# Kernel optimization log

Measured on AMD Instinct MI355X. Metric: run time of the kernel, lower is better.

Reference implementation:

```python
import jax, jax.numpy as jnp
import numpy as np

DT = 0.01        # base_dt from __init__
DT_SCALE = 1.0   # forward default


def setup_inputs() -> dict:
    key = jax.random.key(0)
    k1, k2, k3, k4, k5 = jax.random.split(key, 5)
    B, D, R = 4096, 512, 128
    x = jax.random.normal(k1, (B, D), dtype=jnp.float32)
    v = jax.random.normal(k2, (B, D), dtype=jnp.float32)
    force = jax.random.normal(k3, (B, D), dtype=jnp.float32)
    U = jax.random.normal(k4, (D, R), dtype=jnp.float32) * (1.0 / np.sqrt(D))
    W = jax.random.normal(k5, (R, D), dtype=jnp.float32) * (1.0 / np.sqrt(R))
    return {"x": x, "v": v, "force": force, "U": U, "W": W, "steps": 8}


def reference(x, v, force, U, W, steps):
    dt = DT * DT_SCALE
    # Dormand-Prince (DP5) tableau
    a21 = 1/5
    a31, a32 = 3/40, 9/40
    a41, a42, a43 = 44/45, -56/15, 32/9
    a51, a52, a53, a54 = 19372/6561, -25360/2187, 64448/6561, -212/729
    a61, a62, a63, a64, a65 = 9017/3168, -355/33, 46732/5247, 49/176, -5103/18656
    b1, b3, b4, b5, b6 = 35/384, 500/1113, 125/192, -2187/6784, 11/84

    def dynamics(tx, tv):
        # low-rank Christoffel: gamma(v, x) = ((v @ U) * (x @ U)) @ W
        acc = -jnp.einsum('br,rd->bd', (tv @ U) * (tx @ U), W)
        return acc + force

    def step(carry, _):
        cx, cv = carry
        k1x = cv
        k1v = dynamics(cx, cv)
        x2 = cx + dt * (a21 * k1x); v2 = cv + dt * (a21 * k1v)
        k2x = v2; k2v = dynamics(x2, v2)
        x3 = cx + dt * (a31 * k1x + a32 * k2x)
        v3 = cv + dt * (a31 * k1v + a32 * k2v)
        k3x = v3; k3v = dynamics(x3, v3)
        x4 = cx + dt * (a41 * k1x + a42 * k2x + a43 * k3x)
        v4 = cv + dt * (a41 * k1v + a42 * k2v + a43 * k3v)
        k4x = v4; k4v = dynamics(x4, v4)
        x5 = cx + dt * (a51 * k1x + a52 * k2x + a53 * k3x + a54 * k4x)
        v5 = cv + dt * (a51 * k1v + a52 * k2v + a53 * k3v + a54 * k4v)
        k5x = v5; k5v = dynamics(x5, v5)
        x6 = cx + dt * (a61 * k1x + a62 * k2x + a63 * k3x + a64 * k4x + a65 * k5x)
        v6 = cv + dt * (a61 * k1v + a62 * k2v + a63 * k3v + a64 * k4v + a65 * k5v)
        k6x = v6; k6v = dynamics(x6, v6)
        nx = cx + dt * (b1 * k1x + b3 * k3x + b4 * k4x + b5 * k5x + b6 * k6x)
        nv = cv + dt * (b1 * k1v + b3 * k3v + b4 * k4v + b5 * k5v + b6 * k6v)
        return (nx, nv), None

    (fx, fv), _ = jax.lax.scan(step, (x, v), None, length=steps)
    return fx, fv
```

## Files before the change

kernel.cpp:

```cpp
#include <hip/hip_runtime.h>


typedef _Float16 v8h __attribute__((ext_vector_type(8)));
typedef float v4f __attribute__((ext_vector_type(4)));
typedef unsigned short u16;
typedef unsigned int u32;

#define MFMAH __builtin_amdgcn_mfma_f32_16x16x32_f16
#define INV2048 4.8828125e-4f
#define INV256  0.00390625f
#define SSTR 144

__device__ __forceinline__ float swap8(float x){
  return __int_as_float(
    __builtin_amdgcn_mov_dpp(__float_as_int(x), 0x128, 0xf, 0xf, true));
}

struct Tab {
  double a[7][7]; double b[7]; double A[7]; double XC[7][7]; double XF[7]; double cxc[7];
};
static constexpr Tab make_tab() {
  Tab t{};
  t.a[2][1]=1.0/5;
  t.a[3][1]=3.0/40;       t.a[3][2]=9.0/40;
  t.a[4][1]=44.0/45;      t.a[4][2]=-56.0/15;      t.a[4][3]=32.0/9;
  t.a[5][1]=19372.0/6561; t.a[5][2]=-25360.0/2187; t.a[5][3]=64448.0/6561; t.a[5][4]=-212.0/729;
  t.a[6][1]=9017.0/3168;  t.a[6][2]=-355.0/33;     t.a[6][3]=46732.0/5247; t.a[6][4]=49.0/176; t.a[6][5]=-5103.0/18656;
  t.b[1]=35.0/384; t.b[2]=0.0; t.b[3]=500.0/1113; t.b[4]=125.0/192; t.b[5]=-2187.0/6784; t.b[6]=11.0/84;
  for (int i=1;i<=6;++i){ double s=0; for(int j=1;j<i;++j) s+=t.a[i][j]; t.A[i]=s; }
  for (int i=1;i<=6;++i) for(int l=1;l<i;++l){ double s=0; for(int j=l+1;j<i;++j) s+=t.a[i][j]*t.a[j][l]; t.XC[i][l]=s; }
  for (int i=1;i<=6;++i){ double s=0; for(int j=1;j<i;++j) s+=t.a[i][j]*t.A[j]; t.XF[i]=s; }
  for (int j=1;j<=6;++j){ double s=0; for (int i=j+1;i<=6;++i) s+=t.b[i]*t.a[i][j]; t.cxc[j]=s; }
  return t;
}
static constexpr Tab TB = make_tab();

__device__ __forceinline__ int decode_steps(const void* p){
  int v = *(const int*)p;
  if (v >= 1 && v <= 512) return v;
  float f = *(const float*)p;
  if (f >= 1.f && f <= 512.f) return (int)f;
  return 8;
}
__device__ __forceinline__ void split2s(float x, _Float16& h, _Float16& l){
  h = (_Float16)x;
  l = (_Float16)((x - (float)h) * 2048.0f);
}

#define WS_GH 0
#define WS_GL 16384
#define WS_UH 32768
#define WS_UL 98304
#define WS_WH 163840
#define WS_WL 229376

__global__ __launch_bounds__(512) void k_prep(const float* __restrict__ Ug,
                                              const float* __restrict__ Wg,
                                              _Float16* __restrict__ ws){
  const int tid = threadIdx.x;
  if (blockIdx.x >= 8) {
    int t = (blockIdx.x - 8)*512 + tid;
    if (t < 65536) {
      int r = t >> 7, c = t & 127;
      _Float16 h, l; split2s(Ug[t]*256.f, h, l);
      int kb=r>>5, q2=(r>>3)&3, j=r&7, n2=c>>4, cl=c&15;
      int slot = ((n2*16+kb)*64 + q2*16+cl)*8 + j;
      ws[WS_UH + slot] = h; ws[WS_UL + slot] = l;
    } else {
      int idx = t - 65536;
      int r = idx >> 9, c = idx & 511;
      _Float16 h, l; split2s(Wg[idx]*256.f, h, l);
      int kb=r>>5, q2=(r>>3)&3, j=r&7, n2=c>>4, cl=c&15;
      int slot = ((n2*4+kb)*64 + q2*16+cl)*8 + j;
      ws[WS_WH + slot] = h; ws[WS_WL + slot] = l;
    }
  } else {
    const int b = blockIdx.x;
    const int ww = tid >> 6, lane = tid & 63, q = lane >> 4, c16 = lane & 15;
    const int nb = ww;
    v4f aH = {0,0,0,0}, aC0 = {0,0,0,0}, aC1 = {0,0,0,0};
    #pragma unroll
    for (int kb = 0; kb < 16; ++kb) {
      const float* wp = Wg + (b*16 + c16)*512 + kb*32 + q*8;
      float4 w0 = *(const float4*)wp;
      float4 w1 = *(const float4*)(wp + 4);
      float wv[8] = {w0.x,w0.y,w0.z,w0.w, w1.x,w1.y,w1.z,w1.w};
      v8h Ah, Al, Bh, Bl;
      #pragma unroll
      for (int j = 0; j < 8; ++j) {
        _Float16 h, l; split2s(-wv[j], h, l);
        Ah[j] = h; Al[j] = l;
        float uv = Ug[(kb*32 + q*8 + j)*128 + nb*16 + c16] * 256.f;
        split2s(uv, h, l);
        Bh[j] = h; Bl[j] = l;
      }
      aH = MFMAH(Ah, Bh, aH, 0,0,0);
      if (kb & 1) {
        aC1 = MFMAH(Ah, Bl, aC1, 0,0,0);
        aC1 = MFMAH(Al, Bh, aC1, 0,0,0);
      } else {
        aC0 = MFMAH(Ah, Bl, aC0, 0,0,0);
        aC0 = MFMAH(Al, Bh, aC0, 0,0,0);
      }
    }
    #pragma unroll
    for (int r = 0; r < 4; ++r) {
      float g = aH[r] + (aC0[r] + aC1[r])*INV2048;
      _Float16 h, l; split2s(g, h, l);
      int m = b*16 + 4*q + r, n = nb*16 + c16;
      int slot = (((n>>4)*4 + (m>>5))*64 + ((m>>3)&3)*16 + (n&15))*8 + (m&7);
      ws[WS_GH + slot] = h; ws[WS_GL + slot] = l;
    }
  }
}

#define ARENA 49920

__global__ __launch_bounds__(512,4) void dp5_main(
    const float* __restrict__ xg, const float* __restrict__ vg,
    const float* __restrict__ fg, const void* stepsp,
    const _Float16* __restrict__ ws, float* __restrict__ outg)
{
  __shared__ __align__(16) char arena[ARENA];
  _Float16* base = (_Float16*)arena;
  const _Float16* uH = ws + WS_UH;
  const _Float16* uL = ws + WS_UL;
  const _Float16* wH = ws + WS_WH;
  const _Float16* wL = ws + WS_WL;

  const int tid  = threadIdx.x;
  const int ww   = tid >> 6;
  const int lane = tid & 63;
  const int q    = lane >> 4;
  const int c16  = lane & 15;
  const int nb   = ww;
  const int kcol = nb*16 + c16;
  const int srcl = (q>>1)*16 + c16;
  const bool odd = (q & 1);
  const int rb   = blockIdx.x * 8;
  const int S    = decode_steps(stepsp);
  const float dt = 0.01f;
  const int  brow = c16 & 7;
  const bool hiC  = (c16 >= 8);
  const int  kc0  = nb*16 + 4*q + (hiC ? 2 : 0);

  v8h Gh[4], Gl[4];
  #pragma unroll
  for (int kb = 0; kb < 4; ++kb) {
    int off = ((nb*4 + kb)*64 + lane)*8;
    Gh[kb] = *(const v8h*)(ws + WS_GH + off);
    Gl[kb] = *(const v8h*)(ws + WS_GL + off);
  }

  _Float16* tH = base;
  _Float16* tL = base + 12480;
  const int r16 = tid >> 5, c0 = (tid & 31)*16;
  float xU0[2], vU0[2], fU0[2];
  {
    {
      const float* sp = (r16 < 8) ? (xg + (rb + r16)*512) : (vg + (rb + r16 - 8)*512);
      sp += c0;
      float4 g0 = *(const float4*)(sp);
      float4 g1 = *(const float4*)(sp + 4);
      float4 g2 = *(const float4*)(sp + 8);
      float4 g3 = *(const float4*)(sp + 12);
      float vals[16] = {g0.x,g0.y,g0.z,g0.w, g1.x,g1.y,g1.z,g1.w,
                        g2.x,g2.y,g2.z,g2.w, g3.x,g3.y,g3.z,g3.w};
      v8h vh0, vh1, vl0, vl1;
      #pragma unroll
      for (int j = 0; j < 8; ++j) {
        _Float16 h, l;
        split2s(vals[j], h, l);     vh0[j] = h; vl0[j] = l;
        split2s(vals[8+j], h, l);   vh1[j] = h; vl1[j] = l;
      }
      int o = r16*520 + c0;
      *(v8h*)(tH + o) = vh0; *(v8h*)(tH + o + 8) = vh1;
      *(v8h*)(tL + o) = vl0; *(v8h*)(tL + o + 8) = vl1;
    }
    if (r16 < 8) {
      const float* sp = fg + (rb + r16)*512 + c0;
      float4 g0 = *(const float4*)(sp);
      float4 g1 = *(const float4*)(sp + 4);
      float4 g2 = *(const float4*)(sp + 8);
      float4 g3 = *(const float4*)(sp + 12);
      float vals[16] = {g0.x,g0.y,g0.z,g0.w, g1.x,g1.y,g1.z,g1.w,
                        g2.x,g2.y,g2.z,g2.w, g3.x,g3.y,g3.z,g3.w};
      v8h vh0, vh1, vl0, vl1;
      #pragma unroll
      for (int j = 0; j < 8; ++j) {
        _Float16 h, l;
        split2s(vals[j], h, l);     vh0[j] = h; vl0[j] = l;
        split2s(vals[8+j], h, l);   vh1[j] = h; vl1[j] = l;
      }
      int o = (16 + r16)*520 + c0;
      *(v8h*)(tH + o) = vh0; *(v8h*)(tH + o + 8) = vh1;
      *(v8h*)(tL + o) = vl0; *(v8h*)(tL + o + 8) = vl1;
    }
    __syncthreads();

    v4f aH0={0,0,0,0}, aH1={0,0,0,0}, aC0={0,0,0,0}, aC1={0,0,0,0};
    v4f bH0={0,0,0,0}, bH1={0,0,0,0}, bC0={0,0,0,0}, bC1={0,0,0,0};
    const int arow1 = (c16 < 8) ? (16 + c16) : c16;
    #pragma unroll
    for (int kb = 0; kb < 16; ++kb) {
      int ao0 = c16*520 + kb*32 + q*8;
      int ao1 = arow1*520 + kb*32 + q*8;
      v8h Ah0 = *(const v8h*)(tH + ao0);
      v8h Al0 = *(const v8h*)(tL + ao0);
      v8h Ah1 = *(const v8h*)(tH + ao1);
      v8h Al1 = *(const v8h*)(tL + ao1);
      int bo = ((nb*16 + kb)*64 + lane)*8;
      v8h Bh = *(const v8h*)(uH + bo);
      v8h Bl = *(const v8h*)(uL + bo);
      if (kb & 1) {
        aH1 = MFMAH(Ah0, Bh, aH1, 0,0,0);
        aC1 = MFMAH(Ah0, Bl, aC1, 0,0,0);
        aC1 = MFMAH(Al0, Bh, aC1, 0,0,0);
        bH1 = MFMAH(Ah1, Bh, bH1, 0,0,0);
        bC1 = MFMAH(Ah1, Bl, bC1, 0,0,0);
        bC1 = MFMAH(Al1, Bh, bC1, 0,0,0);
      } else {
        aH0 = MFMAH(Ah0, Bh, aH0, 0,0,0);
        aC0 = MFMAH(Ah0, Bl, aC0, 0,0,0);
        aC0 = MFMAH(Al0, Bh, aC0, 0,0,0);
        bH0 = MFMAH(Ah1, Bh, bH0, 0,0,0);
        bC0 = MFMAH(Ah1, Bl, bC0, 0,0,0);
        bC0 = MFMAH(Al1, Bh, bC0, 0,0,0);
      }
    }
    float at0 = ((aH0[0]+aH1[0]) + (aC0[0]+aC1[0])*INV2048)*INV256;
    float at1 = ((aH0[1]+aH1[1]) + (aC0[1]+aC1[1])*INV2048)*INV256;
    float at2 = ((aH0[2]+aH1[2]) + (aC0[2]+aC1[2])*INV2048)*INV256;
    float at3 = ((aH0[3]+aH1[3]) + (aC0[3]+aC1[3])*INV2048)*INV256;
    float bt0 = ((bH0[0]+bH1[0]) + (bC0[0]+bC1[0])*INV2048)*INV256;
    float bt1 = ((bH0[1]+bH1[1]) + (bC0[1]+bC1[1])*INV2048)*INV256;
    float bt2 = ((bH0[2]+bH1[2]) + (bC0[2]+bC1[2])*INV2048)*INV256;
    float bt3 = ((bH0[3]+bH1[3]) + (bC0[3]+bC1[3])*INV2048)*INV256;
    {
      float sx0=__shfl(at0,srcl,64), sx1=__shfl(at1,srcl,64);
      float sx2=__shfl(at2,srcl,64), sx3=__shfl(at3,srcl,64);
      xU0[0] = odd ? sx2 : sx0; xU0[1] = odd ? sx3 : sx1;
      int srclv = srcl + 32;
      float sv0=__shfl(at0,srclv,64), sv1=__shfl(at1,srclv,64);
      float sv2=__shfl(at2,srclv,64), sv3=__shfl(at3,srclv,64);
      vU0[0] = odd ? sv2 : sv0; vU0[1] = odd ? sv3 : sv1;
    }
    {
      float sf0=__shfl(bt0,srcl,64), sf1=__shfl(bt1,srcl,64);
      float sf2=__shfl(bt2,srcl,64), sf3=__shfl(bt3,srcl,64);
      fU0[0] = odd ? sf2 : sf0; fU0[1] = odd ? sf3 : sf1;
    }
    __syncthreads();
  }

  float cxU2[2], cvU2[2], fU2[2];
  {
    float* T = (float*)arena;
    #pragma unroll
    for (int p2 = 0; p2 < 3; ++p2) {
      float i0 = (p2==0) ? xU0[0] : (p2==1) ? vU0[0] : fU0[0];
      float i1 = (p2==0) ? xU0[1] : (p2==1) ? vU0[1] : fU0[1];
      T[(2*q + 0)*132 + kcol] = i0;
      T[(2*q + 1)*132 + kcol] = i1;
      __syncthreads();
      float2 t2 = *(const float2*)(T + brow*132 + kc0);
      float* o = (p2==0) ? cxU2 : (p2==1) ? cvU2 : fU2;
      o[0] = t2.x; o[1] = t2.y;
      __syncthreads();
    }
  }

  float kU6[6][2], Rr2[2], QXa2[2];
  #pragma unroll
  for (int j = 0; j < 2; ++j) {
    Rr2[j] = 0.f; QXa2[j] = 0.f;
    #pragma unroll
    for (int l = 0; l < 6; ++l) kU6[l][j] = 0.f;
  }

  int pb = 0;
  for (int s = 0; s < S; ++s) {
    float accX[2], accV[2], Pbs[2], Pxcs[2];
    #pragma unroll
    for (int j = 0; j < 2; ++j) { accX[j]=0.f; accV[j]=0.f; Pbs[j]=0.f; Pxcs[j]=0.f; }

    #pragma unroll
    for (int i = 1; i <= 6; ++i) {
      _Float16* bT = base + (pb ? 2304 : 0);
      const float dtA   = dt*(float)TB.A[i];
      const float dt2XF = dt*dt*(float)TB.XF[i];
      const float bi    = (float)TB.b[i];
      const float ci    = (float)TB.cxc[i];
      {
        union { _Float16 h[2]; u32 u; } ph, pl;
        #pragma unroll
        for (int j2 = 0; j2 < 2; ++j2) {
          float vv = cvU2[j2] + dtA*fU2[j2];
          float xx = cxU2[j2] + dtA*cvU2[j2] + dt2XF*fU2[j2];
          #pragma unroll
          for (int l = 1; l < i; ++l) {
            vv += (dt*(float)TB.a[i][l]) * kU6[l-1][j2];
            xx += (dt*dt*(float)TB.XC[i][l]) * kU6[l-1][j2];
          }
          float p = vv*xx;
          Pbs[j2] += bi*p; Pxcs[j2] += ci*p;
          _Float16 h, l2; split2s(p, h, l2);
          ph.h[j2] = h; pl.h[j2] = l2;
        }
        *(u32*)(bT + brow*SSTR + kc0)       = ph.u;
        *(u32*)(bT + (8+brow)*SSTR + kc0)   = pl.u;
      }
      __syncthreads();
      const _Float16* bp = bT + c16*SSTR + q*8;
      v8h B0 = *(const v8h*)(bp);
      v8h B1 = *(const v8h*)(bp + 32);
      v8h B2 = *(const v8h*)(bp + 64);
      v8h B3 = *(const v8h*)(bp + 96);
      v4f C1 = {0,0,0,0}, C2 = {0,0,0,0};
      C1 = MFMAH(Gh[0], B0, C1, 0,0,0);  C2 = MFMAH(Gl[0], B0, C2, 0,0,0);
      C1 = MFMAH(Gh[1], B1, C1, 0,0,0);  C2 = MFMAH(Gl[1], B1, C2, 0,0,0);
      C1 = MFMAH(Gh[2], B2, C1, 0,0,0);  C2 = MFMAH(Gl[2], B2, C2, 0,0,0);
      C1 = MFMAH(Gh[3], B3, C1, 0,0,0);  C2 = MFMAH(Gl[3], B3, C2, 0,0,0);
      float kv[4];
      #pragma unroll
      for (int r = 0; r < 4; ++r) {
        float oth = swap8(C1[r]);
        kv[r] = (C1[r] + (oth + C2[r])*INV2048)*INV256;
      }
      float k2 = swap8(kv[2]);
      float k3 = swap8(kv[3]);
      float kva = hiC ? k2 : kv[0];
      float kvb = hiC ? k3 : kv[1];
      kU6[i-1][0] = kva; kU6[i-1][1] = kvb;
      accX[0] += ci*kva; accV[0] += bi*kva;
      accX[1] += ci*kvb; accV[1] += bi*kvb;
      pb ^= 1;
    }

    #pragma unroll
    for (int j = 0; j < 2; ++j) {
      float nx = cxU2[j] + dt*cvU2[j] + dt*dt*(accX[j] + 0.5f*fU2[j]);
      cvU2[j] += dt*(accV[j] + fU2[j]);
      cxU2[j]  = nx;
      QXa2[j] += Rr2[j] + Pxcs[j];
      Rr2[j]  += Pbs[j];
    }
  }

  __syncthreads();
  _Float16* RQh = base;
  _Float16* RQl = base + 2176;
  {
    union { _Float16 h[2]; u32 u; } t1, t2, t3, t4;
    #pragma unroll
    for (int j2 = 0; j2 < 2; ++j2) {
      _Float16 h, l;
      split2s(Rr2[j2], h, l);  t1.h[j2] = h; t2.h[j2] = l;
      split2s(QXa2[j2], h, l); t3.h[j2] = h; t4.h[j2] = l;
    }
    *(u32*)(RQh + brow*136 + kc0)     = t1.u;
    *(u32*)(RQl + brow*136 + kc0)     = t2.u;
    *(u32*)(RQh + (8+brow)*136 + kc0) = t3.u;
    *(u32*)(RQl + (8+brow)*136 + kc0) = t4.u;
  }
  __syncthreads();

  float* axs = (float*)(arena + 9216);
  float* abs_ = (float*)(arena + 25600);

  #pragma unroll
  for (int cbi = 0; cbi < 4; ++cbi) {
    int cb = nb*4 + cbi;
    v4f aH={0,0,0,0}, aC0={0,0,0,0}, aC1={0,0,0,0};
    #pragma unroll
    for (int kb = 0; kb < 4; ++kb) {
      int bo = ((cb*4 + kb)*64 + lane)*8;
      v8h Bh = *(const v8h*)(wH + bo);
      v8h Bl = *(const v8h*)(wL + bo);
      int ao = c16*136 + kb*32 + q*8;
      v8h Ah = *(const v8h*)(RQh + ao);
      v8h Al = *(const v8h*)(RQl + ao);
      aH = MFMAH(Ah, Bh, aH, 0,0,0);
      if (kb & 1) {
        aC1 = MFMAH(Ah, Bl, aC1, 0,0,0);
        aC1 = MFMAH(Al, Bh, aC1, 0,0,0);
      } else {
        aC0 = MFMAH(Ah, Bl, aC0, 0,0,0);
        aC0 = MFMAH(Al, Bh, aC0, 0,0,0);
      }
    }
    float r0 = (aH[0] + (aC0[0]+aC1[0])*INV2048)*INV256;
    float r1 = (aH[1] + (aC0[1]+aC1[1])*INV2048)*INV256;
    float r2 = (aH[2] + (aC0[2]+aC1[2])*INV2048)*INV256;
    float r3 = (aH[3] + (aC0[3]+aC1[3])*INV2048)*INV256;
    float o0 = __shfl_xor(r0, 32, 64);
    float o1 = __shfl_xor(r1, 32, 64);
    float o2 = __shfl_xor(r2, 32, 64);
    float o3 = __shfl_xor(r3, 32, 64);
    if (q < 2) {
      float abv[4] = {r0, r1, r2, r3};
      float axv[4] = {o0, o1, o2, o3};
      #pragma unroll
      for (int i4 = 0; i4 < 4; ++i4) {
        int lrow = 4*q + i4;
        int lcol = cb*16 + c16;
        axs[lrow*512 + lcol]  = axv[i4];
        abs_[lrow*512 + lcol] = abv[i4];
      }
    }
  }
  __syncthreads();

  const float Sdt = (float)S * dt;
  #pragma unroll
  for (int half = 0; half < 2; ++half) {
    int flat = half*2048 + tid*4;
    int row  = flat >> 9;
    int col  = flat & 511;
    int go   = (rb + row)*512 + col;
    float4 xv = *(const float4*)(xg + go);
    float4 vv = *(const float4*)(vg + go);
    float4 fv = *(const float4*)(fg + go);
    float4 axf = *(const float4*)(axs + flat);
    float4 abf = *(const float4*)(abs_ + flat);
    float4 o1, o2;
    o1.x = xv.x + Sdt*vv.x + 0.5f*Sdt*Sdt*fv.x - dt*dt*axf.x;
    o1.y = xv.y + Sdt*vv.y + 0.5f*Sdt*Sdt*fv.y - dt*dt*axf.y;
    o1.z = xv.z + Sdt*vv.z + 0.5f*Sdt*Sdt*fv.z - dt*dt*axf.z;
    o1.w = xv.w + Sdt*vv.w + 0.5f*Sdt*Sdt*fv.w - dt*dt*axf.w;
    o2.x = vv.x + Sdt*fv.x - dt*abf.x;
    o2.y = vv.y + Sdt*fv.y - dt*abf.y;
    o2.z = vv.z + Sdt*fv.z - dt*abf.z;
    o2.w = vv.w + Sdt*fv.w - dt*abf.w;
    *(float4*)(outg + go) = o1;
    *(float4*)(outg + 2097152 + go) = o2;
  }
}

extern "C" void kernel_launch(void* const* d_in, const int* in_sizes, int n_in,
                              void* d_out, int out_size, void* d_ws, size_t ws_size,
                              hipStream_t stream) {
  const float* x = (const float*)d_in[0];
  const float* v = (const float*)d_in[1];
  const float* f = (const float*)d_in[2];
  const float* U = (const float*)d_in[3];
  const float* W = (const float*)d_in[4];
  _Float16* ws = (_Float16*)d_ws;

  k_prep<<<dim3(264), dim3(512), 0, stream>>>(U, W, ws);
  dp5_main<<<dim3(512), dim3(512), 0, stream>>>(
      x, v, f, d_in[5], ws, (float*)d_out);
}
```

Baseline: 136.4 us.

## Prefetch U/W fragments, merge transposes, split MFMA chains, stagger block starts

Several unrelated changes land together. The U projection loop becomes a rolled loop that prefetches the next pair of B fragments from global memory, and the W-projection epilogue double-buffers its W fragments in registers. The three-pass LDS transpose is merged into a single pass with one barrier pair, the G fragment load moves later to shorten register live ranges, and the per-stage MFMA chain is split into two independent accumulators with a reworked DPP swap reduction. It also adds an s_sleep for blocks with bit 256 set, apparently to stagger memory traffic, which spends idle cycles and raises register pressure.

```diff
diff --git a/kernel.cpp b/kernel.cpp
--- a/kernel.cpp
+++ b/kernel.cpp
@@ -128,6 +128,8 @@
   const _Float16* wH = ws + WS_WH;
   const _Float16* wL = ws + WS_WL;
 
+  if (blockIdx.x & 256) __builtin_amdgcn_s_sleep(19);
+
   const int tid  = threadIdx.x;
   const int ww   = tid >> 6;
   const int lane = tid & 63;
@@ -143,14 +145,6 @@
   const int  brow = c16 & 7;
   const bool hiC  = (c16 >= 8);
   const int  kc0  = nb*16 + 4*q + (hiC ? 2 : 0);
-
-  v8h Gh[4], Gl[4];
-  #pragma unroll
-  for (int kb = 0; kb < 4; ++kb) {
-    int off = ((nb*4 + kb)*64 + lane)*8;
-    Gh[kb] = *(const v8h*)(ws + WS_GH + off);
-    Gl[kb] = *(const v8h*)(ws + WS_GL + off);
-  }
 
   _Float16* tH = base;
   _Float16* tL = base + 12480;
@@ -201,32 +195,47 @@
     v4f aH0={0,0,0,0}, aH1={0,0,0,0}, aC0={0,0,0,0}, aC1={0,0,0,0};
     v4f bH0={0,0,0,0}, bH1={0,0,0,0}, bC0={0,0,0,0}, bC1={0,0,0,0};
     const int arow1 = (c16 < 8) ? (16 + c16) : c16;
-    #pragma unroll
-    for (int kb = 0; kb < 16; ++kb) {
-      int ao0 = c16*520 + kb*32 + q*8;
-      int ao1 = arow1*520 + kb*32 + q*8;
-      v8h Ah0 = *(const v8h*)(tH + ao0);
-      v8h Al0 = *(const v8h*)(tL + ao0);
-      v8h Ah1 = *(const v8h*)(tH + ao1);
-      v8h Al1 = *(const v8h*)(tL + ao1);
-      int bo = ((nb*16 + kb)*64 + lane)*8;
-      v8h Bh = *(const v8h*)(uH + bo);
-      v8h Bl = *(const v8h*)(uL + bo);
-      if (kb & 1) {
-        aH1 = MFMAH(Ah0, Bh, aH1, 0,0,0);
-        aC1 = MFMAH(Ah0, Bl, aC1, 0,0,0);
-        aC1 = MFMAH(Al0, Bh, aC1, 0,0,0);
-        bH1 = MFMAH(Ah1, Bh, bH1, 0,0,0);
-        bC1 = MFMAH(Ah1, Bl, bC1, 0,0,0);
-        bC1 = MFMAH(Al1, Bh, bC1, 0,0,0);
-      } else {
-        aH0 = MFMAH(Ah0, Bh, aH0, 0,0,0);
-        aC0 = MFMAH(Ah0, Bl, aC0, 0,0,0);
-        aC0 = MFMAH(Al0, Bh, aC0, 0,0,0);
-        bH0 = MFMAH(Ah1, Bh, bH0, 0,0,0);
-        bC0 = MFMAH(Ah1, Bl, bC0, 0,0,0);
-        bC0 = MFMAH(Al1, Bh, bC0, 0,0,0);
-      }
+    const int bbase = (nb*16*64 + lane)*8;
+    v8h Bh_e = *(const v8h*)(uH + bbase);
+    v8h Bl_e = *(const v8h*)(uL + bbase);
+    v8h Bh_o = *(const v8h*)(uH + bbase + 512);
+    v8h Bl_o = *(const v8h*)(uL + bbase + 512);
+    #pragma unroll 1
+    for (int kk = 0; kk < 8; ++kk) {
+      const int nk = (2*kk + 2) & 15;
+      v8h nBh_e = *(const v8h*)(uH + bbase + nk*512);
+      v8h nBl_e = *(const v8h*)(uL + bbase + nk*512);
+      v8h nBh_o = *(const v8h*)(uH + bbase + nk*512 + 512);
+      v8h nBl_o = *(const v8h*)(uL + bbase + nk*512 + 512);
+      {
+        int ao0 = c16*520 + (2*kk)*32 + q*8;
+        int ao1 = arow1*520 + (2*kk)*32 + q*8;
+        v8h Ah0 = *(const v8h*)(tH + ao0);
+        v8h Al0 = *(const v8h*)(tL + ao0);
+        v8h Ah1 = *(const v8h*)(tH + ao1);
+        v8h Al1 = *(const v8h*)(tL + ao1);
+        aH0 = MFMAH(Ah0, Bh_e, aH0, 0,0,0);
+        aC0 = MFMAH(Ah0, Bl_e, aC0, 0,0,0);
+        aC0 = MFMAH(Al0, Bh_e, aC0, 0,0,0);
+        bH0 = MFMAH(Ah1, Bh_e, bH0, 0,0,0);
+        bC0 = MFMAH(Ah1, Bl_e, bC0, 0,0,0);
+        bC0 = MFMAH(Al1, Bh_e, bC0, 0,0,0);
+      }
+      {
+        int ao0 = c16*520 + (2*kk+1)*32 + q*8;
+        int ao1 = arow1*520 + (2*kk+1)*32 + q*8;
+        v8h Ah0 = *(const v8h*)(tH + ao0);
+        v8h Al0 = *(const v8h*)(tL + ao0);
+        v8h Ah1 = *(const v8h*)(tH + ao1);
+        v8h Al1 = *(const v8h*)(tL + ao1);
+        aH1 = MFMAH(Ah0, Bh_o, aH1, 0,0,0);
+        aC1 = MFMAH(Ah0, Bl_o, aC1, 0,0,0);
+        aC1 = MFMAH(Al0, Bh_o, aC1, 0,0,0);
+        bH1 = MFMAH(Ah1, Bh_o, bH1, 0,0,0);
+        bC1 = MFMAH(Ah1, Bl_o, bC1, 0,0,0);
+        bC1 = MFMAH(Al1, Bh_o, bC1, 0,0,0);
+      }
+      Bh_e = nBh_e; Bl_e = nBl_e; Bh_o = nBh_o; Bl_o = nBl_o;
     }
     float at0 = ((aH0[0]+aH1[0]) + (aC0[0]+aC1[0])*INV2048)*INV256;
     float at1 = ((aH0[1]+aH1[1]) + (aC0[1]+aC1[1])*INV2048)*INV256;
@@ -256,18 +265,28 @@
   float cxU2[2], cvU2[2], fU2[2];
   {
     float* T = (float*)arena;
-    #pragma unroll
-    for (int p2 = 0; p2 < 3; ++p2) {
-      float i0 = (p2==0) ? xU0[0] : (p2==1) ? vU0[0] : fU0[0];
-      float i1 = (p2==0) ? xU0[1] : (p2==1) ? vU0[1] : fU0[1];
-      T[(2*q + 0)*132 + kcol] = i0;
-      T[(2*q + 1)*132 + kcol] = i1;
-      __syncthreads();
-      float2 t2 = *(const float2*)(T + brow*132 + kc0);
-      float* o = (p2==0) ? cxU2 : (p2==1) ? cvU2 : fU2;
-      o[0] = t2.x; o[1] = t2.y;
-      __syncthreads();
-    }
+    T[       (2*q+0)*132 + kcol] = xU0[0];
+    T[       (2*q+1)*132 + kcol] = xU0[1];
+    T[1056 + (2*q+0)*132 + kcol] = vU0[0];
+    T[1056 + (2*q+1)*132 + kcol] = vU0[1];
+    T[2112 + (2*q+0)*132 + kcol] = fU0[0];
+    T[2112 + (2*q+1)*132 + kcol] = fU0[1];
+    __syncthreads();
+    float2 tx = *(const float2*)(T +        brow*132 + kc0);
+    float2 tv = *(const float2*)(T + 1056 + brow*132 + kc0);
+    float2 tf = *(const float2*)(T + 2112 + brow*132 + kc0);
+    cxU2[0] = tx.x; cxU2[1] = tx.y;
+    cvU2[0] = tv.x; cvU2[1] = tv.y;
+    fU2[0]  = tf.x; fU2[1]  = tf.y;
+    __syncthreads();
+  }
+
+  v8h Gh[4], Gl[4];
+  #pragma unroll
+  for (int kb = 0; kb < 4; ++kb) {
+    int off = ((nb*4 + kb)*64 + lane)*8;
+    Gh[kb] = *(const v8h*)(ws + WS_GH + off);
+    Gl[kb] = *(const v8h*)(ws + WS_GL + off);
   }
 
   float kU6[6][2], Rr2[2], QXa2[2];
@@ -316,24 +335,31 @@
       v8h B1 = *(const v8h*)(bp + 32);
       v8h B2 = *(const v8h*)(bp + 64);
       v8h B3 = *(const v8h*)(bp + 96);
-      v4f C1 = {0,0,0,0}, C2 = {0,0,0,0};
-      C1 = MFMAH(Gh[0], B0, C1, 0,0,0);  C2 = MFMAH(Gl[0], B0, C2, 0,0,0);
-      C1 = MFMAH(Gh[1], B1, C1, 0,0,0);  C2 = MFMAH(Gl[1], B1, C2, 0,0,0);
-      C1 = MFMAH(Gh[2], B2, C1, 0,0,0);  C2 = MFMAH(Gl[2], B2, C2, 0,0,0);
-      C1 = MFMAH(Gh[3], B3, C1, 0,0,0);  C2 = MFMAH(Gl[3], B3, C2, 0,0,0);
-      float kv[4];
-      #pragma unroll
-      for (int r = 0; r < 4; ++r) {
-        float oth = swap8(C1[r]);
-        kv[r] = (C1[r] + (oth + C2[r])*INV2048)*INV256;
-      }
-      float k2 = swap8(kv[2]);
-      float k3 = swap8(kv[3]);
-      float kva = hiC ? k2 : kv[0];
-      float kvb = hiC ? k3 : kv[1];
-      kU6[i-1][0] = kva; kU6[i-1][1] = kvb;
-      accX[0] += ci*kva; accV[0] += bi*kva;
-      accX[1] += ci*kvb; accV[1] += bi*kvb;
+      v4f C1a = {0,0,0,0}, C2a = {0,0,0,0};
+      v4f C1b = {0,0,0,0}, C2b = {0,0,0,0};
+      C1a = MFMAH(Gh[0], B0, C1a, 0,0,0);  C2a = MFMAH(Gl[0], B0, C2a, 0,0,0);
+      C1b = MFMAH(Gh[1], B1, C1b, 0,0,0);  C2b = MFMAH(Gl[1], B1, C2b, 0,0,0);
+      C1a = MFMAH(Gh[2], B2, C1a, 0,0,0);  C2a = MFMAH(Gl[2], B2, C2a, 0,0,0);
+      C1b = MFMAH(Gh[3], B3, C1b, 0,0,0);  C2b = MFMAH(Gl[3], B3, C2b, 0,0,0);
+      {
+        float C1_0 = C1a[0]+C1b[0], C1_1 = C1a[1]+C1b[1];
+        float C1_2 = C1a[2]+C1b[2], C1_3 = C1a[3]+C1b[3];
+        float C2_0 = C2a[0]+C2b[0], C2_1 = C2a[1]+C2b[1];
+        float C2_2 = C2a[2]+C2b[2], C2_3 = C2a[3]+C2b[3];
+        float sa0 = swap8(C1_0), sa2 = swap8(C1_2), sc2 = swap8(C2_2);
+        float sb1 = swap8(C1_1), sb3 = swap8(C1_3), sd3 = swap8(C2_3);
+        float m_a = hiC ? sa2  : C1_0;
+        float n_a = hiC ? C1_2 : sa0;
+        float c_a = hiC ? sc2  : C2_0;
+        float m_b = hiC ? sb3  : C1_1;
+        float n_b = hiC ? C1_3 : sb1;
+        float c_b = hiC ? sd3  : C2_1;
+        float kva = (m_a + (n_a + c_a)*INV2048)*INV256;
+        float kvb = (m_b + (n_b + c_b)*INV2048)*INV256;
+        kU6[i-1][0] = kva; kU6[i-1][1] = kvb;
+        accX[0] += ci*kva; accV[0] += bi*kva;
+        accX[1] += ci*kvb; accV[1] += bi*kvb;
+      }
       pb ^= 1;
     }
 
@@ -363,6 +389,13 @@
     *(u32*)(RQh + (8+brow)*136 + kc0) = t3.u;
     *(u32*)(RQl + (8+brow)*136 + kc0) = t4.u;
   }
+  v8h WAh[4], WAl[4], WBh[4], WBl[4];
+  #pragma unroll
+  for (int kb = 0; kb < 4; ++kb) {
+    int bo = (((nb*4 + 0)*4 + kb)*64 + lane)*8;
+    WAh[kb] = *(const v8h*)(wH + bo);
+    WAl[kb] = *(const v8h*)(wL + bo);
+  }
   __syncthreads();
 
   float* axs = (float*)(arena + 9216);
@@ -371,12 +404,28 @@
   #pragma unroll
   for (int cbi = 0; cbi < 4; ++cbi) {
     int cb = nb*4 + cbi;
+    if (cbi < 3) {
+      if ((cbi & 1) == 0) {
+        #pragma unroll
+        for (int kb = 0; kb < 4; ++kb) {
+          int bo = (((nb*4 + cbi + 1)*4 + kb)*64 + lane)*8;
+          WBh[kb] = *(const v8h*)(wH + bo);
+          WBl[kb] = *(const v8h*)(wL + bo);
+        }
+      } else {
+        #pragma unroll
+        for (int kb = 0; kb < 4; ++kb) {
+          int bo = (((nb*4 + cbi + 1)*4 + kb)*64 + lane)*8;
+          WAh[kb] = *(const v8h*)(wH + bo);
+          WAl[kb] = *(const v8h*)(wL + bo);
+        }
+      }
+    }
     v4f aH={0,0,0,0}, aC0={0,0,0,0}, aC1={0,0,0,0};
     #pragma unroll
     for (int kb = 0; kb < 4; ++kb) {
-      int bo = ((cb*4 + kb)*64 + lane)*8;
-      v8h Bh = *(const v8h*)(wH + bo);
-      v8h Bl = *(const v8h*)(wL + bo);
+      v8h Bh = ((cbi & 1) == 0) ? WAh[kb] : WBh[kb];
+      v8h Bl = ((cbi & 1) == 0) ? WAl[kb] : WBl[kb];
       int ao = c16*136 + kb*32 + q*8;
       v8h Ah = *(const v8h*)(RQh + ao);
       v8h Al = *(const v8h*)(RQl + ao);
```

Measured after the change: 137.1 us. Within noise of the previous version (+0.5%).
